# Optimization experiments

Hardware: AMD Instinct MI355X
Metric: run time of the kernel (lower is better)

The kernel has to match this reference:

```python
import jax, jax.numpy as jnp
import numpy as np

BATCH, NSTEPS, IN_F, OUT_F = 8192, 16, 256, 512


def setup_inputs() -> dict:
    key = jax.random.key(0)
    ks = jax.random.split(key, 20)
    r = jax.random.normal
    return {
        "x": r(ks[0], (BATCH, NSTEPS, IN_F), jnp.float32),
        "C": r(ks[1], (BATCH, OUT_F, 1), jnp.float32),
        "H": r(ks[2], (BATCH, OUT_F, 1), jnp.float32),
        "fg_w_c": r(ks[3], (OUT_F, 1), jnp.float32),
        "fg_w_h": r(ks[4], (OUT_F, OUT_F), jnp.float32),
        "fg_w_x": r(ks[5], (OUT_F, IN_F), jnp.float32),
        "fg_b": r(ks[6], (OUT_F, 1), jnp.float32),
        "ig_w_c": r(ks[7], (OUT_F, 1), jnp.float32),
        "ig_w_h": r(ks[8], (OUT_F, OUT_F), jnp.float32),
        "ig_w_x": r(ks[9], (OUT_F, IN_F), jnp.float32),
        "ig_b": r(ks[10], (OUT_F, 1), jnp.float32),
        "in_w_h": r(ks[11], (OUT_F, OUT_F), jnp.float32),
        "in_w_x": r(ks[12], (OUT_F, IN_F), jnp.float32),
        "in_b": r(ks[13], (OUT_F, 1), jnp.float32),
        "og_w_cn": r(ks[14], (OUT_F, 1), jnp.float32),
        "og_w_h": r(ks[15], (OUT_F, OUT_F), jnp.float32),
        "og_w_x": r(ks[16], (OUT_F, IN_F), jnp.float32),
        "og_b": r(ks[17], (OUT_F, 1), jnp.float32),
        "n": 3,
    }


def reference(x, C, H,
              fg_w_c, fg_w_h, fg_w_x, fg_b,
              ig_w_c, ig_w_h, ig_w_x, ig_b,
              in_w_h, in_w_x, in_b,
              og_w_cn, og_w_h, og_w_x, og_b,
              n):
    # x: [B, T, IN] -> current step [B, IN, 1]
    x_cur = x[:, n, :, None]
    # peephole LSTM gates; matmul broadcasts [O,O] @ [B,O,1] -> [B,O,1]
    fg = jax.nn.sigmoid(fg_w_c * C + jnp.matmul(fg_w_h, H) + jnp.matmul(fg_w_x, x_cur) + fg_b)
    ig = jax.nn.sigmoid(ig_w_c * C + jnp.matmul(ig_w_h, H) + jnp.matmul(ig_w_x, x_cur) + ig_b)
    inn = jnp.tanh(jnp.matmul(in_w_h, H) + jnp.matmul(in_w_x, x_cur) + in_b)
    cm = fg * C + ig * inn
    og = jax.nn.sigmoid(og_w_cn * cm + jnp.matmul(og_w_h, H) + jnp.matmul(og_w_x, x_cur) + og_b)
    h = og * jnp.tanh(cm)
    return (cm, h)
```

## Files before the change

kernel.cpp:

```cpp
#include <hip/hip_runtime.h>


typedef _Float16 half8 __attribute__((ext_vector_type(8)));
typedef _Float16 half4v __attribute__((ext_vector_type(4)));
typedef float floatx4 __attribute__((ext_vector_type(4)));

#define BATCH 8192
#define NSTEPS 16
#define IN_F 256
#define OUT_F 512
#define KDIM 768
#define NDIM 2048
#define HSIZE ((size_t)BATCH * OUT_F)

#define BM 256
#define BN 256
#define BK 64
#define NKT (KDIM / BK)

__device__ __forceinline__ void async_copy16(const void* gptr, void* lptr) {
  __builtin_amdgcn_global_load_lds(
      (const __attribute__((address_space(1))) unsigned int*)gptr,
      (__attribute__((address_space(3))) unsigned int*)lptr,
      16, 0, 0);
}

__device__ __forceinline__ float sigmoidf_(float x) {
  return 1.0f / (1.0f + __expf(-x));
}

__device__ __forceinline__ float tanhf_(float x) {
  x = fminf(fmaxf(x, -20.0f), 20.0f);
  float e = __expf(2.0f * x);
  return (e - 1.0f) / (e + 1.0f);
}

#define PACK_ROWS 8
__global__ void pack_AW(const float* __restrict__ H, const float* __restrict__ x,
                        const int* __restrict__ nptr,
                        const float* __restrict__ fg_w_h, const float* __restrict__ fg_w_x,
                        const float* __restrict__ ig_w_h, const float* __restrict__ ig_w_x,
                        const float* __restrict__ in_w_h, const float* __restrict__ in_w_x,
                        const float* __restrict__ og_w_h, const float* __restrict__ og_w_x,
                        _Float16* __restrict__ A, _Float16* __restrict__ W) {
  const int k = threadIdx.x * 4;
  const int n = *nptr;
  const int row0 = blockIdx.x * PACK_ROWS;
#pragma unroll
  for (int rr = 0; rr < PACK_ROWS; ++rr) {
    const int blk = row0 + rr;
    const float* src;
    _Float16* dst;
    if (blk < BATCH) {
      const int b = blk;
      if (k < OUT_F) {
        src = H + (size_t)b * OUT_F + k;
      } else {
        src = x + ((size_t)b * NSTEPS + n) * IN_F + (k - OUT_F);
      }
      dst = A + (size_t)b * KDIM + k;
    } else {
      const int row = blk - BATCH;
      const int g  = (row >> 4) & 3;
      const int jj = ((row >> 6) << 4) | (row & 15);
      if (k < OUT_F) {
        const float* wh = (g == 0) ? fg_w_h : (g == 1) ? ig_w_h : (g == 2) ? in_w_h : og_w_h;
        src = wh + (size_t)jj * OUT_F + k;
      } else {
        const float* wx = (g == 0) ? fg_w_x : (g == 1) ? ig_w_x : (g == 2) ? in_w_x : og_w_x;
        src = wx + (size_t)jj * IN_F + (k - OUT_F);
      }
      dst = W + (size_t)row * KDIM + k;
    }
    float4 v = *(const float4*)src;
    half4v h = {(_Float16)v.x, (_Float16)v.y, (_Float16)v.z, (_Float16)v.w};
    *(half4v*)dst = h;
  }
}

__global__ __launch_bounds__(512, 2) void gemm_lstm(
    const _Float16* __restrict__ A, const _Float16* __restrict__ W,
    const float* __restrict__ C,
    const float* __restrict__ fg_w_c, const float* __restrict__ fg_b,
    const float* __restrict__ ig_w_c, const float* __restrict__ ig_b,
    const float* __restrict__ in_b,
    const float* __restrict__ og_w_cn, const float* __restrict__ og_b,
    float* __restrict__ out) {
  __shared__ __align__(16) char smem[131072];

  const int tid = threadIdx.x;
  const int lane = tid & 63;
  const int wave = tid >> 6;
  const int quad = lane >> 4;
  const int l16 = lane & 15;
  const int wm = wave >> 2;
  const int wn = wave & 3;

  const int bid = blockIdx.x;
  const int swz = (bid & 7) * 32 + (bid >> 3);
  const int bx = swz & 7;
  const int by = swz >> 3;
  const int m0 = by * BM;
  const int n0 = bx * BN;

  const int jj = (((n0 + wn * 64) >> 6) << 4) | l16;
  const float fwc = fg_w_c[jj], fb = fg_b[jj];
  const float iwc = ig_w_c[jj], ib = ig_b[jj];
  const float nb  = in_b[jj];
  const float owc = og_w_cn[jj], ob = og_b[jj];

  floatx4 acc[8][4] = {};

  auto stage = [&](int p, int t) {
    _Float16* As = (_Float16*)(smem + p * 65536);
    _Float16* Bs = (_Float16*)(smem + p * 65536 + 32768);
    const int kt = t * BK;
#pragma unroll
    for (int r = 0; r < 4; ++r) {
      const int g = r * 512 + tid;
      const int row = g >> 3;
      const int cl = g & 7;
      const int cg = cl ^ (row & 7);
      async_copy16(A + (size_t)(m0 + row) * KDIM + kt + cg * 8, As + g * 8);
      async_copy16(W + (size_t)(n0 + row) * KDIM + kt + cg * 8, Bs + g * 8);
    }
  };

  stage(0, 0);

  for (int t = 0; t < NKT; ++t) {
    if (t + 1 < NKT) {
      stage((t + 1) & 1, t + 1);
      asm volatile("s_waitcnt vmcnt(8)" ::: "memory");
    } else {
      asm volatile("s_waitcnt vmcnt(0)" ::: "memory");
    }
    asm volatile("s_barrier" ::: "memory");

    const _Float16* As = (const _Float16*)(smem + (t & 1) * 65536);
    const _Float16* Bs = (const _Float16*)(smem + (t & 1) * 65536 + 32768);

    half8 bf[4];
#pragma unroll
    for (int ks = 0; ks < 2; ++ks) {
#pragma unroll
      for (int ih = 0; ih < 2; ++ih) {
        if (ih == 0) {
#pragma unroll
          for (int j = 0; j < 4; ++j) {
            const int row = wn * 64 + j * 16 + l16;
            const int chunk = ks * 4 + quad;
            const int gran = row * 8 + (chunk ^ (row & 7));
            bf[j] = *(const half8*)(Bs + gran * 8);
          }
        }
        half8 af[4];
#pragma unroll
        for (int i = 0; i < 4; ++i) {
          const int row = wm * 128 + (ih * 4 + i) * 16 + l16;
          const int chunk = ks * 4 + quad;
          const int gran = row * 8 + (chunk ^ (row & 7));
          af[i] = *(const half8*)(As + gran * 8);
        }
        asm volatile("s_barrier" ::: "memory");
        __builtin_amdgcn_s_setprio(1);
#pragma unroll
        for (int i = 0; i < 4; ++i)
#pragma unroll
          for (int j = 0; j < 4; ++j)
            acc[ih * 4 + i][j] = __builtin_amdgcn_mfma_f32_16x16x32_f16(
                af[i], bf[j], acc[ih * 4 + i][j], 0, 0, 0);
        __builtin_amdgcn_s_setprio(0);
      }
    }
    asm volatile("s_barrier" ::: "memory");
  }

  float* cmS = (float*)smem;
  float* hS  = (float*)(smem + 65536);

  const int jjloc = wn * 16 + l16;
#pragma unroll
  for (int i = 0; i < 8; ++i) {
    const int rbase = m0 + wm * 128 + i * 16 + quad * 4;
    float cv[4];
#pragma unroll
    for (int r = 0; r < 4; ++r)
      cv[r] = C[(size_t)(rbase + r) * OUT_F + jj];
#pragma unroll
    for (int r = 0; r < 4; ++r) {
      const float c = cv[r];
      const float inn = tanhf_(acc[i][2][r] + nb);
      const float fg  = sigmoidf_(fwc * c + acc[i][0][r] + fb);
      const float ig  = sigmoidf_(iwc * c + acc[i][1][r] + ib);
      const float cm  = fg * c + ig * inn;
      const float og  = sigmoidf_(owc * cm + acc[i][3][r] + ob);
      const int rloc = wm * 128 + i * 16 + quad * 4 + r;
      cmS[rloc * 64 + jjloc] = cm;
      hS [rloc * 64 + jjloc] = og * tanhf_(cm);
    }
  }
  __syncthreads();

  const int ub = bx * 64;
#pragma unroll
  for (int q = 0; q < 8; ++q) {
    const int idx = q * 512 + tid;
    const int row = idx >> 4;
    const int c4 = idx & 15;
    const size_t gbase = (size_t)(m0 + row) * OUT_F + ub + c4 * 4;
    *(float4*)(out + gbase) = *(const float4*)(cmS + row * 64 + c4 * 4);
    *(float4*)(out + HSIZE + gbase) = *(const float4*)(hS + row * 64 + c4 * 4);
  }
}

extern "C" void kernel_launch(void* const* d_in, const int* in_sizes, int n_in,
                              void* d_out, int out_size, void* d_ws, size_t ws_size,
                              hipStream_t stream) {
  const float* x       = (const float*)d_in[0];
  const float* C       = (const float*)d_in[1];
  const float* H       = (const float*)d_in[2];
  const float* fg_w_c  = (const float*)d_in[3];
  const float* fg_w_h  = (const float*)d_in[4];
  const float* fg_w_x  = (const float*)d_in[5];
  const float* fg_b    = (const float*)d_in[6];
  const float* ig_w_c  = (const float*)d_in[7];
  const float* ig_w_h  = (const float*)d_in[8];
  const float* ig_w_x  = (const float*)d_in[9];
  const float* ig_b    = (const float*)d_in[10];
  const float* in_w_h  = (const float*)d_in[11];
  const float* in_w_x  = (const float*)d_in[12];
  const float* in_b    = (const float*)d_in[13];
  const float* og_w_cn = (const float*)d_in[14];
  const float* og_w_h  = (const float*)d_in[15];
  const float* og_w_x  = (const float*)d_in[16];
  const float* og_b    = (const float*)d_in[17];
  const int*   nptr    = (const int*)d_in[18];

  char* ws = (char*)d_ws;
  _Float16* Apk = (_Float16*)ws;
  _Float16* Wpk = (_Float16*)(ws + 12582912);
  (void)ws_size; (void)in_sizes; (void)n_in; (void)out_size;

  pack_AW<<<(BATCH + NDIM) / PACK_ROWS, 192, 0, stream>>>(
      H, x, nptr,
      fg_w_h, fg_w_x, ig_w_h, ig_w_x,
      in_w_h, in_w_x, og_w_h, og_w_x,
      Apk, Wpk);
  gemm_lstm<<<dim3(256), 512, 0, stream>>>(Apk, Wpk, C,
                                           fg_w_c, fg_b, ig_w_c, ig_b, in_b,
                                           og_w_cn, og_b, (float*)d_out);
}
```

Before: 261.2 us.

## Split GEMM K-tile loads into half-tiles interleaved across MFMA phases

```diff
diff --git a/kernel.cpp b/kernel.cpp
--- a/kernel.cpp
+++ b/kernel.cpp
@@ -111,69 +111,68 @@
 
   floatx4 acc[8][4] = {};
 
-  auto stage = [&](int p, int t) {
-    _Float16* As = (_Float16*)(smem + p * 65536);
-    _Float16* Bs = (_Float16*)(smem + p * 65536 + 32768);
-    const int kt = t * BK;
-#pragma unroll
-    for (int r = 0; r < 4; ++r) {
-      const int g = r * 512 + tid;
-      const int row = g >> 3;
-      const int cl = g & 7;
-      const int cg = cl ^ (row & 7);
-      async_copy16(A + (size_t)(m0 + row) * KDIM + kt + cg * 8, As + g * 8);
-      async_copy16(W + (size_t)(n0 + row) * KDIM + kt + cg * 8, Bs + g * 8);
+  auto stageU = [&](int X, int mat, int ks) {
+    const _Float16* src = mat ? W : A;
+    const int gb = mat ? n0 : m0;
+    char* base = smem + (X & 1) * 65536 + mat * 32768 + ks * 16384;
+    const int kt = X * BK + ks * 32;
+#pragma unroll
+    for (int g = 0; g < 2; ++g) {
+      const int Ll = g * 512 + tid;
+      const int row = Ll >> 2;
+      const int c2 = (Ll & 3) ^ ((row & 3) ^ ((row >> 2) & 3));
+      async_copy16(src + (size_t)(gb + row) * KDIM + kt + c2 * 8,
+                   base + Ll * 16);
     }
   };
 
-  stage(0, 0);
-
+  stageU(0, 0, 0); stageU(0, 1, 0); stageU(0, 0, 1);
+  stageU(0, 1, 1); stageU(1, 0, 0); stageU(1, 1, 0);
+  asm volatile("s_waitcnt vmcnt(8)" ::: "memory");
+  asm volatile("s_barrier" ::: "memory");
+
+#pragma unroll 2
   for (int t = 0; t < NKT; ++t) {
-    if (t + 1 < NKT) {
-      stage((t + 1) & 1, t + 1);
-      asm volatile("s_waitcnt vmcnt(8)" ::: "memory");
-    } else {
-      asm volatile("s_waitcnt vmcnt(0)" ::: "memory");
-    }
-    asm volatile("s_barrier" ::: "memory");
-
     const _Float16* As = (const _Float16*)(smem + (t & 1) * 65536);
     const _Float16* Bs = (const _Float16*)(smem + (t & 1) * 65536 + 32768);
-
-    half8 bf[4];
-#pragma unroll
-    for (int ks = 0; ks < 2; ++ks) {
-#pragma unroll
-      for (int ih = 0; ih < 2; ++ih) {
-        if (ih == 0) {
-#pragma unroll
-          for (int j = 0; j < 4; ++j) {
-            const int row = wn * 64 + j * 16 + l16;
-            const int chunk = ks * 4 + quad;
-            const int gran = row * 8 + (chunk ^ (row & 7));
-            bf[j] = *(const half8*)(Bs + gran * 8);
-          }
-        }
-        half8 af[4];
-#pragma unroll
-        for (int i = 0; i < 4; ++i) {
-          const int row = wm * 128 + (ih * 4 + i) * 16 + l16;
-          const int chunk = ks * 4 + quad;
-          const int gran = row * 8 + (chunk ^ (row & 7));
-          af[i] = *(const half8*)(As + gran * 8);
-        }
-        asm volatile("s_barrier" ::: "memory");
-        __builtin_amdgcn_s_setprio(1);
-#pragma unroll
-        for (int i = 0; i < 4; ++i)
-#pragma unroll
-          for (int j = 0; j < 4; ++j)
-            acc[ih * 4 + i][j] = __builtin_amdgcn_mfma_f32_16x16x32_f16(
-                af[i], bf[j], acc[ih * 4 + i][j], 0, 0, 0);
-        __builtin_amdgcn_s_setprio(0);
-      }
-    }
-    asm volatile("s_barrier" ::: "memory");
+#pragma unroll
+    for (int ph = 0; ph < 4; ++ph) {
+      const int ks = ph >> 1, mh = ph & 1;
+      half8 af[4], bf[4];
+#pragma unroll
+      for (int j = 0; j < 4; ++j) {
+        const int row = wn * 64 + j * 16 + l16;
+        const int L = ks * 1024 + row * 4 + (quad ^ ((row & 3) ^ ((row >> 2) & 3)));
+        bf[j] = *(const half8*)(Bs + L * 8);
+      }
+#pragma unroll
+      for (int i = 0; i < 4; ++i) {
+        const int row = wm * 128 + (mh * 4 + i) * 16 + l16;
+        const int L = ks * 1024 + row * 4 + (quad ^ ((row & 3) ^ ((row >> 2) & 3)));
+        af[i] = *(const half8*)(As + L * 8);
+      }
+      if (ph == 0)      { if (t + 1 < NKT) stageU(t + 1, 0, 1); }
+      else if (ph == 1) { if (t + 1 < NKT) stageU(t + 1, 1, 1); }
+      else if (ph == 2) { if (t + 2 < NKT) stageU(t + 2, 0, 0); }
+      else              { if (t + 2 < NKT) stageU(t + 2, 1, 0); }
+      asm volatile("s_barrier" ::: "memory");
+      __builtin_amdgcn_s_setprio(1);
+#pragma unroll
+      for (int i = 0; i < 4; ++i)
+#pragma unroll
+        for (int j = 0; j < 4; ++j)
+          acc[mh * 4 + i][j] = __builtin_amdgcn_mfma_f32_16x16x32_f16(
+              af[i], bf[j], acc[mh * 4 + i][j], 0, 0, 0);
+      __builtin_amdgcn_s_setprio(0);
+      if (ph == 1) {
+        if (t < NKT - 1) asm volatile("s_waitcnt vmcnt(8)" ::: "memory");
+        else             asm volatile("s_waitcnt vmcnt(0)" ::: "memory");
+      } else if (ph == 3 && t + 1 < NKT) {
+        if (t + 1 == NKT - 1) asm volatile("s_waitcnt vmcnt(4)" ::: "memory");
+        else                  asm volatile("s_waitcnt vmcnt(8)" ::: "memory");
+      }
+      asm volatile("s_barrier" ::: "memory");
+    }
   }
 
   float* cmS = (float*)smem;
```

New measurement: 264.8 us. Within noise of the previous version (+1.4%).
